# Optimization experiments

Measured on AMD Instinct MI355X. Metric: run time of the kernel, lower is better.

The kernel has to match this reference:

```python
import jax, jax.numpy as jnp
import numpy as np

N_LEVELS = 1024
K = 8  # number of spike timesteps; d/T have length K+1 (index 0 unused)
X_SHAPE = (64, 512, 1024)


def setup_inputs() -> dict:
    key = jax.random.key(0)
    kx, kh0, kh, kd, kT = jax.random.split(key, 5)
    x = jax.random.normal(kx, X_SHAPE, dtype=jnp.float32) * 2.0
    # h: [N_LEVELS, K+1]; column 0 is the sorted search grid (required by searchsorted)
    h0 = jnp.sort(jax.random.uniform(kh0, (N_LEVELS,), minval=-4.0, maxval=4.0))
    h = jax.random.normal(kh, (N_LEVELS, K + 1), dtype=jnp.float32)
    h = h.at[:, 0].set(h0)
    d = jax.random.uniform(kd, (K + 1,), minval=0.05, maxval=1.0)
    T = jax.random.uniform(kT, (K + 1,), minval=-1.0, maxval=1.0)
    b = jnp.float32(0.1)
    return {"x": x, "h": h, "d": d, "T": T, "b": b}


def reference(x, h, d, T, b):
    sp = x.shape
    xf = x.reshape(-1)
    grid = h[:, 0]  # sorted lookup grid
    n = grid.shape[0]
    idx = jnp.clip(jnp.searchsorted(grid, xf), 1, n - 1)
    left = grid[idx - 1]
    right = grid[idx]
    take_left = jnp.abs(xf - left) < jnp.abs(xf - right)
    nearest = jnp.where(take_left, left, right)          # quantized input
    nidx = jnp.where(take_left, idx - 1, idx)            # per-element row into h
    kmax = d.shape[0] - 1
    v = nearest
    out = jnp.zeros_like(xf)
    # loop over the small fixed number of thresholds (data dims fully vectorized)
    for t in range(1, kmax + 1):
        z = (v - T[t] >= 0).astype(xf.dtype)
        out = out + z * d[t]
        if t != kmax:
            v = h[nidx, t + 1]  # irregular per-element gather
    out = out - b
    return out.reshape(sp)
```

## Files before the change

kernel.cpp:

```cpp
#include <hip/hip_runtime.h>
#include <math.h>

#define NL 1024
#define KP1 9

__global__ __launch_bounds__(256) void build_table_kernel(
    const float* __restrict__ h,
    const float* __restrict__ d,
    const float* __restrict__ T,
    const float* __restrict__ bp,
    float* __restrict__ table)
{
    int i = blockIdx.x * blockDim.x + threadIdx.x;
    if (i >= NL) return;
    float v = h[i * KP1 + 0];
    float out = 0.0f;
    float b = bp[0];
#pragma unroll
    for (int t = 1; t <= 8; ++t) {
        float z = ((v - T[t]) >= 0.0f) ? 1.0f : 0.0f;
        out = out + z * d[t];
        if (t != 8) v = h[i * KP1 + (t + 1)];
    }
    table[i] = out - b;
}

__device__ __forceinline__ int swz(int i) { return i + (i >> 5); }

__global__ __launch_bounds__(256) void ps_act_kernel(
    const float* __restrict__ x,
    const float* __restrict__ h,
    const float* __restrict__ table,
    float* __restrict__ out,
    int n4)
{
    __shared__ float  sg[NL + NL / 32];
    __shared__ float4 qd[NL];

    for (int i = threadIdx.x; i < NL; i += blockDim.x) {
        float g = h[i * KP1];
        sg[swz(i)] = g;
        float gm1 = (i > 0) ? h[(i - 1) * KP1] : 0.0f;
        float tm1 = (i > 0) ? table[i - 1] : 0.0f;
        qd[i] = make_float4(gm1, g, tm1, table[i]);
    }
    __syncthreads();

    const float4* __restrict__ x4 = (const float4*)x;
    float4* __restrict__ o4 = (float4*)out;
    const int stride = gridDim.x * blockDim.x;

    for (int i4 = blockIdx.x * blockDim.x + threadIdx.x; i4 < n4; i4 += stride) {
        float4 xv = x4[i4];
        float xin[4] = {xv.x, xv.y, xv.z, xv.w};
        float xo[4];
#pragma unroll
        for (int e = 0; e < 4; ++e) {
            float xf = xin[e];
            int lo = 0;
#pragma unroll
            for (int s = 512; s >= 1; s >>= 1) {
                float v = sg[swz(lo + s - 1)];
                if (v < xf) lo += s;
            }
            int idx = lo < 1 ? 1 : (lo > NL - 1 ? NL - 1 : lo);
            float4 q = qd[idx];
            float dl = fabsf(xf - q.x);
            float dr = fabsf(xf - q.y);
            xo[e] = (dl < dr) ? q.z : q.w;
        }
        o4[i4] = make_float4(xo[0], xo[1], xo[2], xo[3]);
    }
}

extern "C" void kernel_launch(void* const* d_in, const int* in_sizes, int n_in,
                              void* d_out, int out_size, void* d_ws, size_t ws_size,
                              hipStream_t stream) {
    const float* x = (const float*)d_in[0];
    const float* h = (const float*)d_in[1];
    const float* d = (const float*)d_in[2];
    const float* T = (const float*)d_in[3];
    const float* b = (const float*)d_in[4];
    float* out = (float*)d_out;
    float* table = (float*)d_ws;

    int n = in_sizes[0];
    int n4 = n / 4;

    build_table_kernel<<<(NL + 255) / 256, 256, 0, stream>>>(h, d, T, b, table);

    ps_act_kernel<<<2048, 256, 0, stream>>>(x, h, table, out, n4);
}
```

Before: 256.1 us.

## Replace per-element binary search with bucketed decision-boundary lookup

Precomputes the exact float midpoint boundaries between adjacent grid levels, using a bisection over ordered float bit patterns in a single-block build kernel. It then builds an 8192-entry uniform bucket index into those boundaries. The main kernel maps each x to a bucket with one multiply, then scans forward a few boundaries and reads the output table. This replaces the 10-step shared-memory binary search and nearest-neighbor comparison. The costs are a serial one-block preprocessing kernel, more shared memory per block (reducing occupancy), and a data-dependent linear scan that diverges across threads; the grid size is also doubled.

```diff
diff --git a/kernel.cpp b/kernel.cpp
--- a/kernel.cpp
+++ b/kernel.cpp
@@ -1,73 +1,129 @@
 #include <hip/hip_runtime.h>
 #include <math.h>
 
-#define NL 1024
+#define NL  1024
 #define KP1 9
+#define NB  8192
 
-__global__ __launch_bounds__(256) void build_table_kernel(
-    const float* __restrict__ h,
-    const float* __restrict__ d,
-    const float* __restrict__ T,
-    const float* __restrict__ bp,
-    float* __restrict__ table)
-{
-    int i = blockIdx.x * blockDim.x + threadIdx.x;
-    if (i >= NL) return;
-    float v = h[i * KP1 + 0];
-    float out = 0.0f;
-    float b = bp[0];
-#pragma unroll
-    for (int t = 1; t <= 8; ++t) {
-        float z = ((v - T[t]) >= 0.0f) ? 1.0f : 0.0f;
-        out = out + z * d[t];
-        if (t != 8) v = h[i * KP1 + (t + 1)];
-    }
-    table[i] = out - b;
+#define WS_TAB 4
+#define WS_BS  1028
+#define WS_BKT 2060
+
+__device__ __forceinline__ unsigned oi(float f) {
+    unsigned u = __float_as_uint(f);
+    return (u & 0x80000000u) ? ~u : (u | 0x80000000u);
+}
+__device__ __forceinline__ float unoi(unsigned k) {
+    return __uint_as_float((k & 0x80000000u) ? (k & 0x7fffffffu) : ~k);
 }
 
-__device__ __forceinline__ int swz(int i) { return i + (i >> 5); }
+__device__ __forceinline__ int bidx(float x, float lo0, float inv) {
+    float t = (x - lo0) * inv;
+    int j = (int)t;
+    j = j < 0 ? 0 : j;
+    j = j > (NB - 1) ? (NB - 1) : j;
+    return j;
+}
+
+__global__ __launch_bounds__(1024) void build_kernel(
+    const float* __restrict__ h, const float* __restrict__ d,
+    const float* __restrict__ T, const float* __restrict__ bp,
+    float* __restrict__ ws)
+{
+    __shared__ float s_g[NL];
+    __shared__ float s_B[NL];
+    __shared__ int   s_jb[NL];
+    __shared__ float s_lo0, s_inv;
+
+    const int tid = threadIdx.x;
+    float g = h[tid * KP1];
+    s_g[tid] = g;
+
+    {
+        float v = g, outv = 0.0f, b = bp[0];
+#pragma unroll
+        for (int t = 1; t <= 8; ++t) {
+            float z = ((v - T[t]) >= 0.0f) ? 1.0f : 0.0f;
+            outv = outv + z * d[t];
+            if (t != 8) v = h[tid * KP1 + (t + 1)];
+        }
+        ws[WS_TAB + tid] = outv - b;
+    }
+    __syncthreads();
+
+    if (tid < NL - 1) {
+        float l = s_g[tid], r = s_g[tid + 1];
+        unsigned a = oi(l), b2 = oi(r);
+        while (a < b2) {
+            unsigned m = a + ((b2 - a) >> 1);
+            float xm = unoi(m);
+            float dl = fabsf(xm - l), dr = fabsf(xm - r);
+            if (!(dl < dr)) b2 = m; else a = m + 1;
+        }
+        s_B[tid] = unoi(a);
+    } else {
+        s_B[tid] = INFINITY;
+    }
+    __syncthreads();
+
+    if (tid == 0) {
+        float lo0 = s_B[0];
+        float inv = (float)NB / (s_B[NL - 2] - lo0);
+        s_lo0 = lo0; s_inv = inv;
+        ws[0] = lo0; ws[1] = inv;
+    }
+    __syncthreads();
+
+    float lo0 = s_lo0, inv = s_inv;
+    s_jb[tid] = (tid < NL - 1) ? bidx(s_B[tid], lo0, inv) : 0x7fffffff;
+    ws[WS_BS + tid] = s_B[tid];
+    if (tid < 8) ws[WS_BS + NL + tid] = INFINITY;
+    __syncthreads();
+
+    unsigned short* bucket = (unsigned short*)(ws + WS_BKT);
+    for (int j = tid; j < NB; j += 1024) {
+        int lo = 0;
+#pragma unroll
+        for (int s = 512; s >= 1; s >>= 1)
+            if (s_jb[lo + s - 1] < j) lo += s;
+        bucket[j] = (unsigned short)lo;
+    }
+}
 
 __global__ __launch_bounds__(256) void ps_act_kernel(
     const float* __restrict__ x,
-    const float* __restrict__ h,
-    const float* __restrict__ table,
+    const float* __restrict__ ws,
     float* __restrict__ out,
     int n4)
 {
-    __shared__ float  sg[NL + NL / 32];
-    __shared__ float4 qd[NL];
+    __shared__ float          stab[NL];
+    __shared__ float          sBs[NL + 8];
+    __shared__ unsigned short sbk[NB];
 
-    for (int i = threadIdx.x; i < NL; i += blockDim.x) {
-        float g = h[i * KP1];
-        sg[swz(i)] = g;
-        float gm1 = (i > 0) ? h[(i - 1) * KP1] : 0.0f;
-        float tm1 = (i > 0) ? table[i - 1] : 0.0f;
-        qd[i] = make_float4(gm1, g, tm1, table[i]);
-    }
+    const int tid = threadIdx.x;
+    for (int i = tid; i < NL; i += 256)     stab[i] = ws[WS_TAB + i];
+    for (int i = tid; i < NL + 8; i += 256) sBs[i]  = ws[WS_BS + i];
+    const unsigned short* gbk = (const unsigned short*)(ws + WS_BKT);
+    for (int i = tid; i < NB; i += 256)     sbk[i]  = gbk[i];
+    const float lo0 = ws[0];
+    const float inv = ws[1];
     __syncthreads();
 
     const float4* __restrict__ x4 = (const float4*)x;
     float4* __restrict__ o4 = (float4*)out;
     const int stride = gridDim.x * blockDim.x;
 
-    for (int i4 = blockIdx.x * blockDim.x + threadIdx.x; i4 < n4; i4 += stride) {
+    for (int i4 = blockIdx.x * blockDim.x + tid; i4 < n4; i4 += stride) {
         float4 xv = x4[i4];
         float xin[4] = {xv.x, xv.y, xv.z, xv.w};
         float xo[4];
 #pragma unroll
         for (int e = 0; e < 4; ++e) {
             float xf = xin[e];
-            int lo = 0;
-#pragma unroll
-            for (int s = 512; s >= 1; s >>= 1) {
-                float v = sg[swz(lo + s - 1)];
-                if (v < xf) lo += s;
-            }
-            int idx = lo < 1 ? 1 : (lo > NL - 1 ? NL - 1 : lo);
-            float4 q = qd[idx];
-            float dl = fabsf(xf - q.x);
-            float dr = fabsf(xf - q.y);
-            xo[e] = (dl < dr) ? q.z : q.w;
+            int j = bidx(xf, lo0, inv);
+            int ni = sbk[j];
+            while (sBs[ni] <= xf) ++ni;
+            xo[e] = stab[ni];
         }
         o4[i4] = make_float4(xo[0], xo[1], xo[2], xo[3]);
     }
@@ -82,12 +138,11 @@
     const float* T = (const float*)d_in[3];
     const float* b = (const float*)d_in[4];
     float* out = (float*)d_out;
-    float* table = (float*)d_ws;
+    float* ws  = (float*)d_ws;
 
-    int n = in_sizes[0];
+    int n  = in_sizes[0];
     int n4 = n / 4;
 
-    build_table_kernel<<<(NL + 255) / 256, 256, 0, stream>>>(h, d, T, b, table);
-
-    ps_act_kernel<<<2048, 256, 0, stream>>>(x, h, table, out, n4);
+    build_kernel<<<1, 1024, 0, stream>>>(h, d, T, b, ws);
+    ps_act_kernel<<<4096, 256, 0, stream>>>(x, ws, out, n4);
 }
```

Measured after the change: 253.8 us. No clear change (-0.9%).
